# Performance work log

Measured on AMD Instinct MI355X. Metric: run time of the kernel, lower is better.

## Reference

```python
import jax, jax.numpy as jnp
import numpy as np

B, D_IN, H1, H2, LAT, K = 32768, 512, 256, 128, 64, 2048
BN_EPS = 1e-5
COMMIT = 0.25


def _linear_w(k, i, o):
    # xavier-uniform-ish init
    lim = np.sqrt(6.0 / (i + o)).astype(np.float32)
    return jax.random.uniform(k, (i, o), jnp.float32, -lim, lim)


def _bn_params(keys, n):
    g = jax.random.uniform(keys[0], (n,), jnp.float32, 0.5, 1.5)
    b = 0.1 * jax.random.normal(keys[1], (n,), jnp.float32)
    m = 0.1 * jax.random.normal(keys[2], (n,), jnp.float32)
    v = jax.random.uniform(keys[3], (n,), jnp.float32, 0.5, 1.5)
    return g, b, m, v


def setup_inputs() -> dict:
    key = jax.random.key(0)
    ks = jax.random.split(key, 32)
    inp = {"x": jax.random.normal(ks[0], (B, D_IN), jnp.float32)}
    # encoder: 512 -> 256 -> 128 -> 64
    inp["ew1"], inp["eb1"] = _linear_w(ks[1], D_IN, H1), jnp.zeros((H1,), jnp.float32)
    inp["eg1"], inp["ebt1"], inp["em1"], inp["ev1"] = _bn_params(jax.random.split(ks[2], 4), H1)
    inp["ew2"], inp["eb2"] = _linear_w(ks[3], H1, H2), jnp.zeros((H2,), jnp.float32)
    inp["eg2"], inp["ebt2"], inp["em2"], inp["ev2"] = _bn_params(jax.random.split(ks[4], 4), H2)
    inp["ew3"], inp["eb3"] = _linear_w(ks[5], H2, LAT), jnp.zeros((LAT,), jnp.float32)
    # codebook (num_embeddings, latent_dim)
    inp["codebook"] = _linear_w(ks[6], K, LAT).reshape(K, LAT)
    # decoder: 64 -> 128 -> 256 -> 512
    inp["dw1"], inp["db1"] = _linear_w(ks[7], LAT, H2), jnp.zeros((H2,), jnp.float32)
    inp["dg1"], inp["dbt1"], inp["dm1"], inp["dv1"] = _bn_params(jax.random.split(ks[8], 4), H2)
    inp["dw2"], inp["db2"] = _linear_w(ks[9], H2, H1), jnp.zeros((H1,), jnp.float32)
    inp["dg2"], inp["dbt2"], inp["dm2"], inp["dv2"] = _bn_params(jax.random.split(ks[10], 4), H1)
    inp["dw3"], inp["db3"] = _linear_w(ks[11], H1, D_IN), jnp.zeros((D_IN,), jnp.float32)
    return inp


def _bn(x, g, b, m, v):
    # BatchNorm1d in eval mode: running stats
    return (x - m) * (g * jax.lax.rsqrt(v + BN_EPS)) + b


def reference(x, ew1, eb1, eg1, ebt1, em1, ev1,
              ew2, eb2, eg2, ebt2, em2, ev2,
              ew3, eb3, codebook,
              dw1, db1, dg1, dbt1, dm1, dv1,
              dw2, db2, dg2, dbt2, dm2, dv2,
              dw3, db3):
    # ---- encoder MLP (Dropout is identity in eval) ----
    h = _bn(jax.nn.relu(x @ ew1 + eb1), eg1, ebt1, em1, ev1)
    h = _bn(jax.nn.relu(h @ ew2 + eb2), eg2, ebt2, em2, ev2)
    z_e = h @ ew3 + eb3  # [B, LAT]

    # ---- vector quantization: cdist + argmin + gather ----
    # squared L2 distance (argmin-equivalent to cdist p=2)
    d2 = (jnp.sum(z_e * z_e, axis=1, keepdims=True)
          + jnp.sum(codebook * codebook, axis=1)[None, :]
          - 2.0 * (z_e @ codebook.T))  # [B, K]
    idx = jnp.argmin(d2, axis=-1)  # [B]
    z_q = codebook[idx]  # gather, [B, LAT]

    codebook_loss = jnp.mean((z_q - jax.lax.stop_gradient(z_e)) ** 2)
    commit_loss = jnp.mean((z_e - jax.lax.stop_gradient(z_q)) ** 2)
    vq_loss = codebook_loss + COMMIT * commit_loss

    # straight-through estimator
    z_q = z_e + jax.lax.stop_gradient(z_q - z_e)

    # ---- decoder MLP ----
    h = _bn(jax.nn.relu(z_q @ dw1 + db1), dg1, dbt1, dm1, dv1)
    h = _bn(jax.nn.relu(h @ dw2 + db2), dg2, dbt2, dm2, dv2)
    x_recon = h @ dw3 + db3  # [B, D_IN]

    recon_err = jnp.mean((x_recon - x) ** 2)
    return x_recon, vq_loss, idx, recon_err
```

## Files before the change

### kernel.cpp

```cpp
#include <hip/hip_runtime.h>

#define B_ROWS 32768
#define D_IN   512
#define H1_N   256
#define H2_N   128
#define LAT_N  64
#define K_CB   2048

#define BN 128
#define BK 32

#define VQ_MARGIN 4.0e-3f

typedef __attribute__((ext_vector_type(8))) short s8v;
typedef __attribute__((ext_vector_type(4))) float f4v;

__device__ inline unsigned short f2bf(float f) {
    union { float f; unsigned u; } v; v.f = f;
    unsigned r = v.u + 0x7fffu + ((v.u >> 16) & 1u);
    return (unsigned short)(r >> 16);
}
__device__ inline float bf2f(unsigned short h) {
    union { unsigned u; float f; } v; v.u = ((unsigned)h) << 16;
    return v.f;
}

#define SWZ(row) ((((row) >> 2) & 7) << 3)

__global__ __launch_bounds__(128, 2) void gemm_f32_wide(
    const float* __restrict__ A, const float* __restrict__ W,
    const float* __restrict__ bias,
    const float* __restrict__ bn_g, const float* __restrict__ bn_b,
    const float* __restrict__ bn_m, const float* __restrict__ bn_v,
    float* __restrict__ out, int M, int N)
{
    __shared__ float sA[BK][128];
    __shared__ float sB[BK][BN];
    const int tid = threadIdx.x;
    const int tr = tid >> 4;
    const int tc = tid & 15;
    const int row0 = blockIdx.x * 128;
    const int n0   = blockIdx.y * BN;

    float acc[16][8];
#pragma unroll
    for (int i = 0; i < 16; ++i)
#pragma unroll
        for (int j = 0; j < 8; ++j) acc[i][j] = 0.f;

    for (int k0 = 0; k0 < M; k0 += BK) {
#pragma unroll
        for (int it = 0; it < 8; ++it) {
            int s = tid + it * 128;
            int m = s >> 3;
            int kq = s & 7;
            float4 v = *reinterpret_cast<const float4*>(
                &A[(size_t)(row0 + m) * M + k0 + kq * 4]);
            int kk = kq * 4;
            sA[kk + 0][m ^ SWZ(kk + 0)] = v.x;
            sA[kk + 1][m ^ SWZ(kk + 1)] = v.y;
            sA[kk + 2][m ^ SWZ(kk + 2)] = v.z;
            sA[kk + 3][m ^ SWZ(kk + 3)] = v.w;
        }
#pragma unroll
        for (int it = 0; it < 8; ++it) {
            int s = tid + it * 128;
            int k = s >> 5;
            int nq = s & 31;
            float4 v = *reinterpret_cast<const float4*>(
                &W[(size_t)(k0 + k) * N + n0 + nq * 4]);
            *reinterpret_cast<float4*>(&sB[k][nq * 4]) = v;
        }
        __syncthreads();
#pragma unroll 4
        for (int k = 0; k < BK; ++k) {
            int b0a = (tr * 16) ^ SWZ(k);
            int b1a = (tr * 16 + 8) ^ SWZ(k);
            float a[16];
            {
                float4 v0 = *reinterpret_cast<float4*>(&sA[k][b0a]);
                float4 v1 = *reinterpret_cast<float4*>(&sA[k][b0a + 4]);
                float4 v2 = *reinterpret_cast<float4*>(&sA[k][b1a]);
                float4 v3 = *reinterpret_cast<float4*>(&sA[k][b1a + 4]);
                a[0]=v0.x; a[1]=v0.y; a[2]=v0.z; a[3]=v0.w;
                a[4]=v1.x; a[5]=v1.y; a[6]=v1.z; a[7]=v1.w;
                a[8]=v2.x; a[9]=v2.y; a[10]=v2.z; a[11]=v2.w;
                a[12]=v3.x; a[13]=v3.y; a[14]=v3.z; a[15]=v3.w;
            }
            float4 c0 = *reinterpret_cast<float4*>(&sB[k][tc * 4]);
            float4 c1 = *reinterpret_cast<float4*>(&sB[k][64 + tc * 4]);
            float b[8] = {c0.x, c0.y, c0.z, c0.w, c1.x, c1.y, c1.z, c1.w};
#pragma unroll
            for (int i = 0; i < 16; ++i)
#pragma unroll
                for (int j = 0; j < 8; ++j)
                    acc[i][j] = fmaf(a[i], b[j], acc[i][j]);
        }
        __syncthreads();
    }

    const int nb0 = n0 + tc * 4;
    const int nb1 = n0 + 64 + tc * 4;
    float bi[8], sc[8], sh[8];
#pragma unroll
    for (int g = 0; g < 2; ++g) {
        int nb = g ? nb1 : nb0;
#pragma unroll
        for (int j = 0; j < 4; ++j) {
            int n = nb + j;
            bi[g * 4 + j] = bias[n];
            float s = bn_g[n] * rsqrtf(bn_v[n] + 1e-5f);
            sc[g * 4 + j] = s;
            sh[g * 4 + j] = bn_b[n] - bn_m[n] * s;
        }
    }
#pragma unroll
    for (int i = 0; i < 16; ++i) {
        int row = row0 + tr * 16 + i;
#pragma unroll
        for (int g = 0; g < 2; ++g) {
            int nb = g ? nb1 : nb0;
            float o[4];
#pragma unroll
            for (int j = 0; j < 4; ++j) {
                float v = acc[i][g * 4 + j] + bi[g * 4 + j];
                v = v > 0.f ? v : 0.f;
                v = v * sc[g * 4 + j] + sh[g * 4 + j];
                o[j] = v;
            }
            *reinterpret_cast<float4*>(&out[(size_t)row * N + nb]) =
                make_float4(o[0], o[1], o[2], o[3]);
        }
    }
}

template <int MODE>
__global__ __launch_bounds__(256, 6) void gemm_fused(
    const float* __restrict__ A, const float* __restrict__ W,
    const float* __restrict__ bias,
    const float* __restrict__ bn_g, const float* __restrict__ bn_b,
    const float* __restrict__ bn_m, const float* __restrict__ bn_v,
    float* __restrict__ out, int M, int N)
{
    __shared__ float sA[BK][64];
    __shared__ float sB[BK][BN];
    const int tid = threadIdx.x;
    const int tr = tid >> 4;
    const int tc = tid & 15;
    const int row0 = blockIdx.x * 64;
    const int n0   = blockIdx.y * BN;

    float acc[4][8];
#pragma unroll
    for (int i = 0; i < 4; ++i)
#pragma unroll
        for (int j = 0; j < 8; ++j) acc[i][j] = 0.f;

    for (int k0 = 0; k0 < M; k0 += BK) {
#pragma unroll
        for (int it = 0; it < 2; ++it) {
            int s = tid + it * 256;
            int m = s >> 3;
            int kq = s & 7;
            float4 v = *reinterpret_cast<const float4*>(
                &A[(size_t)(row0 + m) * M + k0 + kq * 4]);
            int kk = kq * 4;
            sA[kk + 0][m ^ SWZ(kk + 0)] = v.x;
            sA[kk + 1][m ^ SWZ(kk + 1)] = v.y;
            sA[kk + 2][m ^ SWZ(kk + 2)] = v.z;
            sA[kk + 3][m ^ SWZ(kk + 3)] = v.w;
        }
#pragma unroll
        for (int it = 0; it < 4; ++it) {
            int s = tid + it * 256;
            int k = s >> 5;
            int nq = s & 31;
            int n = n0 + nq * 4;
            float4 v = make_float4(0.f, 0.f, 0.f, 0.f);
            if (n < N)
                v = *reinterpret_cast<const float4*>(&W[(size_t)(k0 + k) * N + n]);
            *reinterpret_cast<float4*>(&sB[k][nq * 4]) = v;
        }
        __syncthreads();
#pragma unroll 4
        for (int k = 0; k < BK; ++k) {
            int ac = (tr * 4) ^ SWZ(k);
            float4 a0 = *reinterpret_cast<float4*>(&sA[k][ac]);
            float a[4] = {a0.x, a0.y, a0.z, a0.w};
            float4 b0 = *reinterpret_cast<float4*>(&sB[k][tc * 4]);
            float4 b1 = *reinterpret_cast<float4*>(&sB[k][64 + tc * 4]);
            float b[8] = {b0.x, b0.y, b0.z, b0.w, b1.x, b1.y, b1.z, b1.w};
#pragma unroll
            for (int i = 0; i < 4; ++i)
#pragma unroll
                for (int j = 0; j < 8; ++j)
                    acc[i][j] = fmaf(a[i], b[j], acc[i][j]);
        }
        __syncthreads();
    }

    const int nb0 = n0 + tc * 4;
    const int nb1 = n0 + 64 + tc * 4;
    float bi[8], sc[8], sh[8];
#pragma unroll
    for (int g = 0; g < 2; ++g) {
        int nb = g ? nb1 : nb0;
        if (nb < N) {
#pragma unroll
            for (int j = 0; j < 4; ++j) {
                int n = nb + j;
                bi[g * 4 + j] = bias[n];
                if (MODE == 0) {
                    float s = bn_g[n] * rsqrtf(bn_v[n] + 1e-5f);
                    sc[g * 4 + j] = s;
                    sh[g * 4 + j] = bn_b[n] - bn_m[n] * s;
                }
            }
        }
    }
#pragma unroll
    for (int i = 0; i < 4; ++i) {
        int row = row0 + tr * 4 + i;
#pragma unroll
        for (int g = 0; g < 2; ++g) {
            int nb = g ? nb1 : nb0;
            if (nb < N) {
                float o[4];
#pragma unroll
                for (int j = 0; j < 4; ++j) {
                    float v = acc[i][g * 4 + j] + bi[g * 4 + j];
                    if (MODE == 0) {
                        v = v > 0.f ? v : 0.f;
                        v = v * sc[g * 4 + j] + sh[g * 4 + j];
                    }
                    o[j] = v;
                }
                *reinterpret_cast<float4*>(&out[(size_t)row * N + nb]) =
                    make_float4(o[0], o[1], o[2], o[3]);
            }
        }
    }
}

__device__ inline void wprep_body(const float* __restrict__ w,
                                  unsigned short* __restrict__ w_hi,
                                  unsigned short* __restrict__ w_lo,
                                  int K, int N, int idx)
{
    if (idx >= N * K) return;
    int n = idx / K, k = idx - n * K;
    float f = w[(size_t)k * N + n];
    unsigned u = __float_as_uint(f);
    float lo = f - __uint_as_float(u & 0xffff0000u);
    w_hi[idx] = (unsigned short)(u >> 16);
    w_lo[idx] = f2bf(lo);
}

__global__ __launch_bounds__(256) void prep_all(
    const float* __restrict__ dw3, unsigned short* w3hi, unsigned short* w3lo,
    const float* __restrict__ dw2, unsigned short* w2hi, unsigned short* w2lo,
    const float* __restrict__ dw1, unsigned short* w1hi, unsigned short* w1lo,
    const float* __restrict__ cb, unsigned short* cb_hi, unsigned short* cb_lo,
    float* __restrict__ cn, int* __restrict__ rcnt, float* __restrict__ repairp)
{
    int bid = blockIdx.x;
    int tid = threadIdx.x;
    if (bid < 512) {
        wprep_body(dw3, w3hi, w3lo, H1_N, D_IN, bid * 256 + tid);
    } else if (bid < 640) {
        wprep_body(dw2, w2hi, w2lo, H2_N, H1_N, (bid - 512) * 256 + tid);
    } else if (bid < 672) {
        wprep_body(dw1, w1hi, w1lo, LAT_N, H2_N, (bid - 640) * 256 + tid);
    } else {
        int blk = bid - 672;
        if (blk == 0) {
            if (tid == 0) rcnt[0] = 0;
            repairp[tid] = 0.f;
        }
        int j = blk * 256 + tid;
        float s = 0.f;
#pragma unroll
        for (int lq = 0; lq < 16; ++lq) {
            float4 v = *reinterpret_cast<const float4*>(&cb[(size_t)j * LAT_N + lq * 4]);
            float e[4] = {v.x, v.y, v.z, v.w};
            ushort4 h, l;
            unsigned short* hp = &h.x;
            unsigned short* lp = &l.x;
#pragma unroll
            for (int t = 0; t < 4; ++t) {
                s = fmaf(e[t], e[t], s);
                unsigned short hb = f2bf(e[t]);
                hp[t] = hb;
                lp[t] = f2bf(e[t] - bf2f(hb));
            }
            *reinterpret_cast<ushort4*>(&cb_hi[(size_t)j * LAT_N + lq * 4]) = h;
            *reinterpret_cast<ushort4*>(&cb_lo[(size_t)j * LAT_N + lq * 4]) = l;
        }
        cn[j] = s;
    }
}

template <int MODE, int K>
__global__ __launch_bounds__(256, 2) void mfma_gemm(
    const unsigned short* __restrict__ A_hi,
    const unsigned short* __restrict__ A_lo,
    const unsigned short* __restrict__ w_hi,
    const unsigned short* __restrict__ w_lo,
    const float* __restrict__ bias,
    const float* __restrict__ bn_g, const float* __restrict__ bn_b,
    const float* __restrict__ bn_m, const float* __restrict__ bn_v,
    unsigned short* __restrict__ out_hi, unsigned short* __restrict__ out_lo,
    float* __restrict__ out_f32,
    const float* __restrict__ xref, float* __restrict__ partials, int N)
{
    const int lane = threadIdx.x & 63;
    const int wv = threadIdx.x >> 6;
    const int wr = wv >> 1, wc = wv & 1;
    const int rbase = blockIdx.x * 128 + wr * 64;
    const int cbase = blockIdx.y * 128 + wc * 64;
    const int lr = lane & 15, lg = lane >> 4;

    f4v acc[4][4];
#pragma unroll
    for (int rt = 0; rt < 4; ++rt)
#pragma unroll
        for (int ct = 0; ct < 4; ++ct)
            acc[rt][ct] = (f4v){0.f, 0.f, 0.f, 0.f};

#pragma unroll
    for (int ks = 0; ks < K / 32; ++ks) {
        s8v ah[4], al[4], bh[4], bl[4];
#pragma unroll
        for (int rt = 0; rt < 4; ++rt) {
            size_t off = (size_t)(rbase + rt * 16 + lr) * K + ks * 32 + lg * 8;
            ah[rt] = *reinterpret_cast<const s8v*>(&A_hi[off]);
            al[rt] = *reinterpret_cast<const s8v*>(&A_lo[off]);
        }
#pragma unroll
        for (int ct = 0; ct < 4; ++ct) {
            size_t off = (size_t)(cbase + ct * 16 + lr) * K + ks * 32 + lg * 8;
            bh[ct] = *reinterpret_cast<const s8v*>(&w_hi[off]);
            bl[ct] = *reinterpret_cast<const s8v*>(&w_lo[off]);
        }
#pragma unroll
        for (int rt = 0; rt < 4; ++rt)
#pragma unroll
            for (int ct = 0; ct < 4; ++ct) {
                acc[rt][ct] = __builtin_amdgcn_mfma_f32_16x16x32_bf16(
                    ah[rt], bh[ct], acc[rt][ct], 0, 0, 0);
                acc[rt][ct] = __builtin_amdgcn_mfma_f32_16x16x32_bf16(
                    al[rt], bh[ct], acc[rt][ct], 0, 0, 0);
                acc[rt][ct] = __builtin_amdgcn_mfma_f32_16x16x32_bf16(
                    ah[rt], bl[ct], acc[rt][ct], 0, 0, 0);
            }
    }

    float sq = 0.f;
#pragma unroll
    for (int ct = 0; ct < 4; ++ct) {
        int col = cbase + ct * 16 + lr;
        float bi = bias[col];
        float sc = 0.f, sh = 0.f;
        if (MODE == 0) {
            float s = bn_g[col] * rsqrtf(bn_v[col] + 1e-5f);
            sc = s;
            sh = bn_b[col] - bn_m[col] * s;
        }
#pragma unroll
        for (int rt = 0; rt < 4; ++rt)
#pragma unroll
            for (int i = 0; i < 4; ++i) {
                int row = rbase + rt * 16 + lg * 4 + i;
                float v = acc[rt][ct][i] + bi;
                if (MODE == 0) {
                    v = fmaxf(v, 0.f) * sc + sh;
                    unsigned u = __float_as_uint(v);
                    out_hi[(size_t)row * N + col] = (unsigned short)(u >> 16);
                    out_lo[(size_t)row * N + col] =
                        f2bf(v - __uint_as_float(u & 0xffff0000u));
                }
                if (MODE == 2) {
                    float d = v - xref[(size_t)row * N + col];
                    sq = fmaf(d, d, sq);
                    out_f32[(size_t)row * N + col] = v;
                }
            }
    }
    if (MODE == 2) {
        __shared__ float red[256];
        red[threadIdx.x] = sq;
        __syncthreads();
        for (int off = 128; off > 0; off >>= 1) {
            if (threadIdx.x < off) red[threadIdx.x] += red[threadIdx.x + off];
            __syncthreads();
        }
        if (threadIdx.x == 0)
            partials[blockIdx.y * gridDim.x + blockIdx.x] = red[0];
    }
}

__global__ __launch_bounds__(256) void vq_mfma(
    const float* __restrict__ z, const unsigned short* __restrict__ cb_hi,
    const unsigned short* __restrict__ cb_lo, const float* __restrict__ cnorm,
    float4* __restrict__ cand)
{
    const int lane = threadIdx.x & 63;
    const int wid  = blockIdx.x * 4 + (threadIdx.x >> 6);
    const int rbase = (wid >> 3) * 64;
    const int cblk  = wid & 7;
    const int cbase = cblk * 256;
    const int lr = lane & 15;
    const int lg = lane >> 4;

    s8v a_hi[4][2], a_lo[4][2];
#pragma unroll
    for (int rt = 0; rt < 4; ++rt) {
        int row = rbase + rt * 16 + lr;
#pragma unroll
        for (int ks = 0; ks < 2; ++ks) {
            const float* p = &z[(size_t)row * LAT_N + ks * 32 + lg * 8];
            float4 v0 = *reinterpret_cast<const float4*>(p);
            float4 v1 = *reinterpret_cast<const float4*>(p + 4);
            float vv[8] = {v0.x, v0.y, v0.z, v0.w, v1.x, v1.y, v1.z, v1.w};
#pragma unroll
            for (int jj = 0; jj < 8; ++jj) {
                unsigned short hb = f2bf(vv[jj]);
                a_hi[rt][ks][jj] = (short)hb;
                a_lo[rt][ks][jj] = (short)f2bf(vv[jj] - bf2f(hb));
            }
        }
    }

    float b1[4][4], b2[4][4];
    int j1[4][4];
#pragma unroll
    for (int rt = 0; rt < 4; ++rt)
#pragma unroll
        for (int i = 0; i < 4; ++i) {
            b1[rt][i] = 3.4e38f; b2[rt][i] = 3.4e38f; j1[rt][i] = 0;
        }

    for (int ct = 0; ct < 16; ++ct) {
        int col = cbase + ct * 16 + lr;
        const unsigned short* ph = &cb_hi[(size_t)col * LAT_N + lg * 8];
        const unsigned short* pl = &cb_lo[(size_t)col * LAT_N + lg * 8];
        s8v bh0 = *reinterpret_cast<const s8v*>(ph);
        s8v bh1 = *reinterpret_cast<const s8v*>(ph + 32);
        s8v bl0 = *reinterpret_cast<const s8v*>(pl);
        s8v bl1 = *reinterpret_cast<const s8v*>(pl + 32);
        float cn = cnorm[col];
#pragma unroll
        for (int rt = 0; rt < 4; ++rt) {
            f4v acc = {0.f, 0.f, 0.f, 0.f};
            acc = __builtin_amdgcn_mfma_f32_16x16x32_bf16(a_hi[rt][0], bh0, acc, 0, 0, 0);
            acc = __builtin_amdgcn_mfma_f32_16x16x32_bf16(a_hi[rt][1], bh1, acc, 0, 0, 0);
            acc = __builtin_amdgcn_mfma_f32_16x16x32_bf16(a_lo[rt][0], bh0, acc, 0, 0, 0);
            acc = __builtin_amdgcn_mfma_f32_16x16x32_bf16(a_lo[rt][1], bh1, acc, 0, 0, 0);
            acc = __builtin_amdgcn_mfma_f32_16x16x32_bf16(a_hi[rt][0], bl0, acc, 0, 0, 0);
            acc = __builtin_amdgcn_mfma_f32_16x16x32_bf16(a_hi[rt][1], bl1, acc, 0, 0, 0);
#pragma unroll
            for (int i = 0; i < 4; ++i) {
                float d = fmaf(-2.f, acc[i], cn);
// ... 68 lines not shown
    float sq = 0.f;
    if (b2 - b1 >= VQ_MARGIN) {
#pragma unroll
        for (int lq = 0; lq < 16; ++lq) {
            float4 cv = *reinterpret_cast<const float4*>(&cb[(size_t)j1 * LAT_N + lq * 4]);
            float4 zv = *reinterpret_cast<const float4*>(&z[(size_t)row * LAT_N + lq * 4]);
            float d0 = cv.x - zv.x, d1 = cv.y - zv.y;
            float d2 = cv.z - zv.z, d3 = cv.w - zv.w;
            sq = fmaf(d0, d0, sq); sq = fmaf(d1, d1, sq);
            sq = fmaf(d2, d2, sq); sq = fmaf(d3, d3, sq);
        }
        const uint4* gh = reinterpret_cast<const uint4*>(&cbhi[(size_t)j1 * LAT_N]);
        const uint4* gl = reinterpret_cast<const uint4*>(&cblo[(size_t)j1 * LAT_N]);
        uint4* dh = reinterpret_cast<uint4*>(&zqhi[(size_t)row * LAT_N]);
        uint4* dl = reinterpret_cast<uint4*>(&zqlo[(size_t)row * LAT_N]);
#pragma unroll
        for (int q = 0; q < 8; ++q) { dh[q] = gh[q]; dl[q] = gl[q]; }
    } else {
        int s = atomicAdd(rcnt, 1);
        if (s < B_ROWS) rlist[s] = row;
    }
    red[tid] = sq;
    __syncthreads();
    for (int off = 128; off > 0; off >>= 1) {
        if (tid < off) red[tid] += red[tid + off];
        __syncthreads();
    }
    if (tid == 0) mergep[blockIdx.x] = red[0];
}

#define RB 8
__global__ __launch_bounds__(256) void vq_repair(
    const int* __restrict__ rcnt, const int* __restrict__ rlist,
    const float* __restrict__ z, const float* __restrict__ cb,
    const float* __restrict__ cn,
    const unsigned short* __restrict__ cbhi,
    const unsigned short* __restrict__ cblo,
    unsigned short* __restrict__ zqhi, unsigned short* __restrict__ zqlo,
    float* __restrict__ idxf, float* __restrict__ repairp)
{
    __shared__ float sz[RB][LAT_N];
    __shared__ float rv[256];
    __shared__ int ri[256];
    const int tid = threadIdx.x;
    const int count = min(rcnt[0], B_ROWS);
    if (blockIdx.x * RB >= count) return;
    float lsum = 0.f;
    for (int base = blockIdx.x * RB; base < count; base += gridDim.x * RB) {
        int nr = min(RB, count - base);
        __syncthreads();
        for (int s = tid; s < nr * LAT_N; s += 256) {
            int r = s >> 6, d = s & 63;
            int rr = rlist[base + r];
            rr = ((unsigned)rr < (unsigned)B_ROWS) ? rr : 0;
            sz[r][d] = z[(size_t)rr * LAT_N + d];
        }
        __syncthreads();
        float bv[RB];
        int bj[RB];
#pragma unroll
        for (int r = 0; r < RB; ++r) { bv[r] = 3.4e38f; bj[r] = 0; }
        for (int k = 0; k < K_CB / 256; ++k) {
            int cidx = tid + k * 256;
            float acc[RB];
#pragma unroll
            for (int r = 0; r < RB; ++r) acc[r] = 0.f;
            const float* cp = &cb[(size_t)cidx * LAT_N];
#pragma unroll 2
            for (int d4 = 0; d4 < 16; ++d4) {
                float4 cv = *reinterpret_cast<const float4*>(cp + d4 * 4);
#pragma unroll
                for (int r = 0; r < RB; ++r) {
                    acc[r] = fmaf(sz[r][d4 * 4 + 0], cv.x, acc[r]);
                    acc[r] = fmaf(sz[r][d4 * 4 + 1], cv.y, acc[r]);
                    acc[r] = fmaf(sz[r][d4 * 4 + 2], cv.z, acc[r]);
                    acc[r] = fmaf(sz[r][d4 * 4 + 3], cv.w, acc[r]);
                }
            }
            float cnv = cn[cidx];
#pragma unroll
            for (int r = 0; r < RB; ++r) {
                float d = fmaf(-2.f, acc[r], cnv);
                if (d < bv[r] || (d == bv[r] && cidx < bj[r])) {
                    bv[r] = d; bj[r] = cidx;
                }
            }
        }
        for (int r = 0; r < RB; ++r) {
            if (r >= nr) break;
            rv[tid] = bv[r];
            ri[tid] = bj[r];
            __syncthreads();
            for (int off = 128; off > 0; off >>= 1) {
                if (tid < off) {
                    float ov = rv[tid + off];
                    int oi = ri[tid + off];
                    if (ov < rv[tid] || (ov == rv[tid] && oi < ri[tid])) {
                        rv[tid] = ov; ri[tid] = oi;
                    }
                }
                __syncthreads();
            }
            int bjf = ri[0];
            int rr = rlist[base + r];
            bool ok = (unsigned)rr < (unsigned)B_ROWS;
            rr = ok ? rr : 0;
            if (tid == 0 && ok) idxf[rr] = (float)bjf;
            float v = 0.f;
            if (tid < 64) {
                float d = cb[(size_t)bjf * LAT_N + tid] - sz[r][tid];
                v = d * d;
            }
            __syncthreads();
            rv[tid] = v;
            __syncthreads();
// ... 77 lines not shown
    const float* dg2  = (const float*)d_in[24];
    const float* dbt2 = (const float*)d_in[25];
    const float* dm2  = (const float*)d_in[26];
    const float* dv2  = (const float*)d_in[27];
    const float* dw3  = (const float*)d_in[28];
    const float* db3  = (const float*)d_in[29];

    float* outf = (float*)d_out;
    const size_t XR_OFF = 0;
    const size_t VQ_OFF = (size_t)B_ROWS * D_IN;
    const size_t IDX_OFF = VQ_OFF + 1;
    const size_t RE_OFF = IDX_OFF + B_ROWS;

    float* wsf = (float*)d_ws;
    size_t off = 0;
    float* buf256 = wsf + off; off += (size_t)B_ROWS * H1_N;
    float* buf128 = wsf + off; off += (size_t)B_ROWS * H2_N;
    float* zbuf   = wsf + off; off += (size_t)B_ROWS * LAT_N;
    float* cnbuf  = wsf + off; off += K_CB;
    float* mergep = wsf + off; off += 128;
    float* repairp= wsf + off; off += 256;
    float* rep    = wsf + off; off += 1024;
    unsigned short* cbhi = (unsigned short*)(wsf + off); off += K_CB * LAT_N / 2;
    unsigned short* cblo = (unsigned short*)(wsf + off); off += K_CB * LAT_N / 2;
    float4* candb = (float4*)(wsf + off); off += (size_t)B_ROWS * 8 * 4;
    int* rcnt  = (int*)(wsf + off); off += 16;
    int* rlist = (int*)(wsf + off); off += B_ROWS;
    unsigned short* w1hi = (unsigned short*)(wsf + off); off += (H2_N * LAT_N) / 2;
    unsigned short* w1lo = (unsigned short*)(wsf + off); off += (H2_N * LAT_N) / 2;
    unsigned short* w2hi = (unsigned short*)(wsf + off); off += (H1_N * H2_N) / 2;
    unsigned short* w2lo = (unsigned short*)(wsf + off); off += (H1_N * H2_N) / 2;
    unsigned short* w3hi = (unsigned short*)(wsf + off); off += (D_IN * H1_N) / 2;
    unsigned short* w3lo = (unsigned short*)(wsf + off); off += (D_IN * H1_N) / 2;
    unsigned short* zqhi = (unsigned short*)(wsf + off); off += (size_t)B_ROWS * LAT_N / 2;
    unsigned short* zqlo = (unsigned short*)(wsf + off); off += (size_t)B_ROWS * LAT_N / 2;

    unsigned short* h1hi = (unsigned short*)buf128;
    unsigned short* h1lo = (unsigned short*)(buf128 + (size_t)B_ROWS * 64);
    unsigned short* h2hi = (unsigned short*)buf256;
    unsigned short* h2lo = (unsigned short*)(buf256 + (size_t)B_ROWS * 128);

    dim3 blk(256);

    prep_all<<<dim3(680), blk, 0, stream>>>(
        dw3, w3hi, w3lo, dw2, w2hi, w2lo, dw1, w1hi, w1lo,
        cb, cbhi, cblo, cnbuf, rcnt, repairp);

    gemm_f32_wide<<<dim3(B_ROWS / 128, H1_N / BN), dim3(128), 0, stream>>>(
        x, ew1, eb1, eg1, ebt1, em1, ev1, buf256, D_IN, H1_N);
    gemm_fused<0><<<dim3(B_ROWS / 64, 1), blk, 0, stream>>>(
        buf256, ew2, eb2, eg2, ebt2, em2, ev2, buf128, H1_N, H2_N);
    gemm_fused<1><<<dim3(B_ROWS / 64, 1), blk, 0, stream>>>(
        buf128, ew3, eb3, nullptr, nullptr, nullptr, nullptr, zbuf, H2_N, LAT_N);

    vq_mfma<<<dim3(1024), blk, 0, stream>>>(zbuf, cbhi, cblo, cnbuf, candb);
    vq_merge<<<dim3(B_ROWS / 256), blk, 0, stream>>>(
        candb, zbuf, cb, cbhi, cblo, zqhi, zqlo,
        outf + IDX_OFF, rlist, rcnt, mergep);
    vq_repair<<<dim3(256), blk, 0, stream>>>(
        rcnt, rlist, zbuf, cb, cnbuf, cbhi, cblo, zqhi, zqlo,
        outf + IDX_OFF, repairp);

    mfma_gemm<0, LAT_N><<<dim3(B_ROWS / 128, H2_N / 128), blk, 0, stream>>>(
        zqhi, zqlo, w1hi, w1lo, db1, dg1, dbt1, dm1, dv1,
        h1hi, h1lo, nullptr, nullptr, nullptr, H2_N);
    mfma_gemm<0, H2_N><<<dim3(B_ROWS / 128, H1_N / 128), blk, 0, stream>>>(
        h1hi, h1lo, w2hi, w2lo, db2, dg2, dbt2, dm2, dv2,
        h2hi, h2lo, nullptr, nullptr, nullptr, H1_N);
    mfma_gemm<2, H1_N><<<dim3(B_ROWS / 128, D_IN / 128), blk, 0, stream>>>(
        h2hi, h2lo, w3hi, w3lo, db3, nullptr, nullptr, nullptr, nullptr,
        nullptr, nullptr, outf + XR_OFF, x, rep, D_IN);

    finalize_kernel<<<dim3(1), blk, 0, stream>>>(
        mergep, 128, repairp, 256, rep, 1024, outf + VQ_OFF, outf + RE_OFF);
}
```

Before: 479.8 us.

## Move encoder GEMMs to split-bf16 MFMA and recompute encoder in repair

Replaces the fp32 FMA encoder GEMMs with the existing MFMA kernel, which uses hi/lo bf16 splitting. The first layer splits x into hi/lo on the fly, and the encoder weights are pre-split in prep_all. The last encoder layer also emits z as hi/lo so vq_mfma consumes it directly. The VQ margin is widened, and the repair kernel now recomputes the encoder exactly in fp32 from x for ambiguous rows, which adds repair work whenever more rows fall inside the margin.

```diff
diff --git a/kernel.cpp b/kernel.cpp
--- a/kernel.cpp
+++ b/kernel.cpp
@@ -7,10 +7,7 @@
 #define LAT_N  64
 #define K_CB   2048
 
-#define BN 128
-#define BK 32
-
-#define VQ_MARGIN 4.0e-3f
+#define VQ_MARGIN 6.0e-3f
 
 typedef __attribute__((ext_vector_type(8))) short s8v;
 typedef __attribute__((ext_vector_type(4))) float f4v;
@@ -25,283 +22,9 @@
     return v.f;
 }
 
-#define SWZ(row) ((((row) >> 2) & 7) << 3)
-
-__global__ __launch_bounds__(128, 2) void gemm_f32_wide(
-    const float* __restrict__ A, const float* __restrict__ W,
-    const float* __restrict__ bias,
-    const float* __restrict__ bn_g, const float* __restrict__ bn_b,
-    const float* __restrict__ bn_m, const float* __restrict__ bn_v,
-    float* __restrict__ out, int M, int N)
-{
-    __shared__ float sA[BK][128];
-    __shared__ float sB[BK][BN];
-    const int tid = threadIdx.x;
-    const int tr = tid >> 4;
-    const int tc = tid & 15;
-    const int row0 = blockIdx.x * 128;
-    const int n0   = blockIdx.y * BN;
-
-    float acc[16][8];
-#pragma unroll
-    for (int i = 0; i < 16; ++i)
-#pragma unroll
-        for (int j = 0; j < 8; ++j) acc[i][j] = 0.f;
-
-    for (int k0 = 0; k0 < M; k0 += BK) {
-#pragma unroll
-        for (int it = 0; it < 8; ++it) {
-            int s = tid + it * 128;
-            int m = s >> 3;
-            int kq = s & 7;
-            float4 v = *reinterpret_cast<const float4*>(
-                &A[(size_t)(row0 + m) * M + k0 + kq * 4]);
-            int kk = kq * 4;
-            sA[kk + 0][m ^ SWZ(kk + 0)] = v.x;
-            sA[kk + 1][m ^ SWZ(kk + 1)] = v.y;
-            sA[kk + 2][m ^ SWZ(kk + 2)] = v.z;
-            sA[kk + 3][m ^ SWZ(kk + 3)] = v.w;
-        }
-#pragma unroll
-        for (int it = 0; it < 8; ++it) {
-            int s = tid + it * 128;
-            int k = s >> 5;
-            int nq = s & 31;
-            float4 v = *reinterpret_cast<const float4*>(
-                &W[(size_t)(k0 + k) * N + n0 + nq * 4]);
-            *reinterpret_cast<float4*>(&sB[k][nq * 4]) = v;
-        }
-        __syncthreads();
-#pragma unroll 4
-        for (int k = 0; k < BK; ++k) {
-            int b0a = (tr * 16) ^ SWZ(k);
-            int b1a = (tr * 16 + 8) ^ SWZ(k);
-            float a[16];
-            {
-                float4 v0 = *reinterpret_cast<float4*>(&sA[k][b0a]);
-                float4 v1 = *reinterpret_cast<float4*>(&sA[k][b0a + 4]);
-                float4 v2 = *reinterpret_cast<float4*>(&sA[k][b1a]);
-                float4 v3 = *reinterpret_cast<float4*>(&sA[k][b1a + 4]);
-                a[0]=v0.x; a[1]=v0.y; a[2]=v0.z; a[3]=v0.w;
-                a[4]=v1.x; a[5]=v1.y; a[6]=v1.z; a[7]=v1.w;
-                a[8]=v2.x; a[9]=v2.y; a[10]=v2.z; a[11]=v2.w;
-                a[12]=v3.x; a[13]=v3.y; a[14]=v3.z; a[15]=v3.w;
-            }
-            float4 c0 = *reinterpret_cast<float4*>(&sB[k][tc * 4]);
-            float4 c1 = *reinterpret_cast<float4*>(&sB[k][64 + tc * 4]);
-            float b[8] = {c0.x, c0.y, c0.z, c0.w, c1.x, c1.y, c1.z, c1.w};
-#pragma unroll
-            for (int i = 0; i < 16; ++i)
-#pragma unroll
-                for (int j = 0; j < 8; ++j)
-                    acc[i][j] = fmaf(a[i], b[j], acc[i][j]);
-        }
-        __syncthreads();
-    }
-
-    const int nb0 = n0 + tc * 4;
-    const int nb1 = n0 + 64 + tc * 4;
-    float bi[8], sc[8], sh[8];
-#pragma unroll
-    for (int g = 0; g < 2; ++g) {
-        int nb = g ? nb1 : nb0;
-#pragma unroll
-        for (int j = 0; j < 4; ++j) {
-            int n = nb + j;
-            bi[g * 4 + j] = bias[n];
-            float s = bn_g[n] * rsqrtf(bn_v[n] + 1e-5f);
-            sc[g * 4 + j] = s;
-            sh[g * 4 + j] = bn_b[n] - bn_m[n] * s;
-        }
-    }
-#pragma unroll
-    for (int i = 0; i < 16; ++i) {
-        int row = row0 + tr * 16 + i;
-#pragma unroll
-        for (int g = 0; g < 2; ++g) {
-            int nb = g ? nb1 : nb0;
-            float o[4];
-#pragma unroll
-            for (int j = 0; j < 4; ++j) {
-                float v = acc[i][g * 4 + j] + bi[g * 4 + j];
-                v = v > 0.f ? v : 0.f;
-                v = v * sc[g * 4 + j] + sh[g * 4 + j];
-                o[j] = v;
-            }
-            *reinterpret_cast<float4*>(&out[(size_t)row * N + nb]) =
-                make_float4(o[0], o[1], o[2], o[3]);
-        }
-    }
-}
-
-template <int MODE>
-__global__ __launch_bounds__(256, 6) void gemm_fused(
-    const float* __restrict__ A, const float* __restrict__ W,
-    const float* __restrict__ bias,
-    const float* __restrict__ bn_g, const float* __restrict__ bn_b,
-    const float* __restrict__ bn_m, const float* __restrict__ bn_v,
-    float* __restrict__ out, int M, int N)
-{
-    __shared__ float sA[BK][64];
-    __shared__ float sB[BK][BN];
-    const int tid = threadIdx.x;
-    const int tr = tid >> 4;
-    const int tc = tid & 15;
-    const int row0 = blockIdx.x * 64;
-    const int n0   = blockIdx.y * BN;
-
-    float acc[4][8];
-#pragma unroll
-    for (int i = 0; i < 4; ++i)
-#pragma unroll
-        for (int j = 0; j < 8; ++j) acc[i][j] = 0.f;
-
-    for (int k0 = 0; k0 < M; k0 += BK) {
-#pragma unroll
-        for (int it = 0; it < 2; ++it) {
-            int s = tid + it * 256;
-            int m = s >> 3;
-            int kq = s & 7;
-            float4 v = *reinterpret_cast<const float4*>(
-                &A[(size_t)(row0 + m) * M + k0 + kq * 4]);
-            int kk = kq * 4;
-            sA[kk + 0][m ^ SWZ(kk + 0)] = v.x;
-            sA[kk + 1][m ^ SWZ(kk + 1)] = v.y;
-            sA[kk + 2][m ^ SWZ(kk + 2)] = v.z;
-            sA[kk + 3][m ^ SWZ(kk + 3)] = v.w;
-        }
-#pragma unroll
-        for (int it = 0; it < 4; ++it) {
-            int s = tid + it * 256;
-            int k = s >> 5;
-            int nq = s & 31;
-            int n = n0 + nq * 4;
-            float4 v = make_float4(0.f, 0.f, 0.f, 0.f);
-            if (n < N)
-                v = *reinterpret_cast<const float4*>(&W[(size_t)(k0 + k) * N + n]);
-            *reinterpret_cast<float4*>(&sB[k][nq * 4]) = v;
-        }
-        __syncthreads();
-#pragma unroll 4
-        for (int k = 0; k < BK; ++k) {
-            int ac = (tr * 4) ^ SWZ(k);
-            float4 a0 = *reinterpret_cast<float4*>(&sA[k][ac]);
-            float a[4] = {a0.x, a0.y, a0.z, a0.w};
-            float4 b0 = *reinterpret_cast<float4*>(&sB[k][tc * 4]);
-            float4 b1 = *reinterpret_cast<float4*>(&sB[k][64 + tc * 4]);
-            float b[8] = {b0.x, b0.y, b0.z, b0.w, b1.x, b1.y, b1.z, b1.w};
-#pragma unroll
-            for (int i = 0; i < 4; ++i)
-#pragma unroll
-                for (int j = 0; j < 8; ++j)
-                    acc[i][j] = fmaf(a[i], b[j], acc[i][j]);
-        }
-        __syncthreads();
-    }
-
-    const int nb0 = n0 + tc * 4;
-    const int nb1 = n0 + 64 + tc * 4;
-    float bi[8], sc[8], sh[8];
-#pragma unroll
-    for (int g = 0; g < 2; ++g) {
-        int nb = g ? nb1 : nb0;
-        if (nb < N) {
-#pragma unroll
-            for (int j = 0; j < 4; ++j) {
-                int n = nb + j;
-                bi[g * 4 + j] = bias[n];
-                if (MODE == 0) {
-                    float s = bn_g[n] * rsqrtf(bn_v[n] + 1e-5f);
-                    sc[g * 4 + j] = s;
-                    sh[g * 4 + j] = bn_b[n] - bn_m[n] * s;
-                }
-            }
-        }
-    }
-#pragma unroll
-    for (int i = 0; i < 4; ++i) {
-        int row = row0 + tr * 4 + i;
-#pragma unroll
-        for (int g = 0; g < 2; ++g) {
-            int nb = g ? nb1 : nb0;
-            if (nb < N) {
-                float o[4];
-#pragma unroll
-                for (int j = 0; j < 4; ++j) {
-                    float v = acc[i][g * 4 + j] + bi[g * 4 + j];
-                    if (MODE == 0) {
-                        v = v > 0.f ? v : 0.f;
-                        v = v * sc[g * 4 + j] + sh[g * 4 + j];
-                    }
-                    o[j] = v;
-                }
-                *reinterpret_cast<float4*>(&out[(size_t)row * N + nb]) =
-                    make_float4(o[0], o[1], o[2], o[3]);
-            }
-        }
-    }
-}
-
-__device__ inline void wprep_body(const float* __restrict__ w,
-                                  unsigned short* __restrict__ w_hi,
-                                  unsigned short* __restrict__ w_lo,
-                                  int K, int N, int idx)
-{
-    if (idx >= N * K) return;
-    int n = idx / K, k = idx - n * K;
-    float f = w[(size_t)k * N + n];
-    unsigned u = __float_as_uint(f);
-    float lo = f - __uint_as_float(u & 0xffff0000u);
-    w_hi[idx] = (unsigned short)(u >> 16);
-    w_lo[idx] = f2bf(lo);
-}
-
-__global__ __launch_bounds__(256) void prep_all(
-    const float* __restrict__ dw3, unsigned short* w3hi, unsigned short* w3lo,
-    const float* __restrict__ dw2, unsigned short* w2hi, unsigned short* w2lo,
-    const float* __restrict__ dw1, unsigned short* w1hi, unsigned short* w1lo,
-    const float* __restrict__ cb, unsigned short* cb_hi, unsigned short* cb_lo,
-    float* __restrict__ cn, int* __restrict__ rcnt, float* __restrict__ repairp)
-{
-    int bid = blockIdx.x;
-    int tid = threadIdx.x;
-    if (bid < 512) {
-        wprep_body(dw3, w3hi, w3lo, H1_N, D_IN, bid * 256 + tid);
-    } else if (bid < 640) {
-        wprep_body(dw2, w2hi, w2lo, H2_N, H1_N, (bid - 512) * 256 + tid);
-    } else if (bid < 672) {
-        wprep_body(dw1, w1hi, w1lo, LAT_N, H2_N, (bid - 640) * 256 + tid);
-    } else {
-        int blk = bid - 672;
-        if (blk == 0) {
-            if (tid == 0) rcnt[0] = 0;
-            repairp[tid] = 0.f;
-        }
-        int j = blk * 256 + tid;
-        float s = 0.f;
-#pragma unroll
-        for (int lq = 0; lq < 16; ++lq) {
-            float4 v = *reinterpret_cast<const float4*>(&cb[(size_t)j * LAT_N + lq * 4]);
-            float e[4] = {v.x, v.y, v.z, v.w};
-            ushort4 h, l;
-            unsigned short* hp = &h.x;
-            unsigned short* lp = &l.x;
-#pragma unroll
-            for (int t = 0; t < 4; ++t) {
-                s = fmaf(e[t], e[t], s);
-                unsigned short hb = f2bf(e[t]);
-                hp[t] = hb;
-                lp[t] = f2bf(e[t] - bf2f(hb));
-            }
-            *reinterpret_cast<ushort4*>(&cb_hi[(size_t)j * LAT_N + lq * 4]) = h;
-            *reinterpret_cast<ushort4*>(&cb_lo[(size_t)j * LAT_N + lq * 4]) = l;
-        }
-        cn[j] = s;
-    }
-}
-
-template <int MODE, int K>
+template <int MODE, int K, int CT, bool ASPLIT>
 __global__ __launch_bounds__(256, 2) void mfma_gemm(
+    const float* __restrict__ A_f32,
     const unsigned short* __restrict__ A_hi,
     const unsigned short* __restrict__ A_lo,
     const unsigned short* __restrict__ w_hi,
@@ -317,27 +40,48 @@
     const int wv = threadIdx.x >> 6;
     const int wr = wv >> 1, wc = wv & 1;
     const int rbase = blockIdx.x * 128 + wr * 64;
-    const int cbase = blockIdx.y * 128 + wc * 64;
+    const int cbase = blockIdx.y * (32 * CT) + wc * (16 * CT);
     const int lr = lane & 15, lg = lane >> 4;
 
-    f4v acc[4][4];
+    f4v acc[4][CT];
 #pragma unroll
     for (int rt = 0; rt < 4; ++rt)
 #pragma unroll
-        for (int ct = 0; ct < 4; ++ct)
+        for (int ct = 0; ct < CT; ++ct)
             acc[rt][ct] = (f4v){0.f, 0.f, 0.f, 0.f};
 
-#pragma unroll
     for (int ks = 0; ks < K / 32; ++ks) {
-        s8v ah[4], al[4], bh[4], bl[4];
+        s8v ah[4], al[4], bh[CT], bl[CT];
 #pragma unroll
         for (int rt = 0; rt < 4; ++rt) {
             size_t off = (size_t)(rbase + rt * 16 + lr) * K + ks * 32 + lg * 8;
-            ah[rt] = *reinterpret_cast<const s8v*>(&A_hi[off]);
-            al[rt] = *reinterpret_cast<const s8v*>(&A_lo[off]);
-        }
-#pragma unroll
-        for (int ct = 0; ct < 4; ++ct) {
+            if constexpr (ASPLIT) {
+                const float* p = &A_f32[off];
+                float4 v0 = *reinterpret_cast<const float4*>(p);
+                float4 v1 = *reinterpret_cast<const float4*>(p + 4);
+                float fv[8] = {v0.x, v0.y, v0.z, v0.w, v1.x, v1.y, v1.z, v1.w};
+                unsigned uu[8], llv[8];
+#pragma unroll
+                for (int j = 0; j < 8; ++j) {
+                    uu[j] = __float_as_uint(fv[j]);
+                    float lo = fv[j] - __uint_as_float(uu[j] & 0xffff0000u);
+                    llv[j] = __float_as_uint(lo);
+                }
+                union { s8v v; unsigned w[4]; } H, L;
+#pragma unroll
+                for (int m = 0; m < 4; ++m) {
+                    H.w[m] = __builtin_amdgcn_perm(uu[2 * m + 1], uu[2 * m], 0x07060302u);
+                    L.w[m] = __builtin_amdgcn_perm(llv[2 * m + 1], llv[2 * m], 0x07060302u);
+                }
+                ah[rt] = H.v;
+                al[rt] = L.v;
+            } else {
+                ah[rt] = *reinterpret_cast<const s8v*>(&A_hi[off]);
+                al[rt] = *reinterpret_cast<const s8v*>(&A_lo[off]);
+            }
+        }
+#pragma unroll
+        for (int ct = 0; ct < CT; ++ct) {
             size_t off = (size_t)(cbase + ct * 16 + lr) * K + ks * 32 + lg * 8;
             bh[ct] = *reinterpret_cast<const s8v*>(&w_hi[off]);
             bl[ct] = *reinterpret_cast<const s8v*>(&w_lo[off]);
@@ -345,7 +89,7 @@
 #pragma unroll
         for (int rt = 0; rt < 4; ++rt)
 #pragma unroll
-            for (int ct = 0; ct < 4; ++ct) {
+            for (int ct = 0; ct < CT; ++ct) {
                 acc[rt][ct] = __builtin_amdgcn_mfma_f32_16x16x32_bf16(
                     ah[rt], bh[ct], acc[rt][ct], 0, 0, 0);
                 acc[rt][ct] = __builtin_amdgcn_mfma_f32_16x16x32_bf16(
@@ -357,7 +101,7 @@
 
     float sq = 0.f;
 #pragma unroll
-    for (int ct = 0; ct < 4; ++ct) {
+    for (int ct = 0; ct < CT; ++ct) {
         int col = cbase + ct * 16 + lr;
         float bi = bias[col];
         float sc = 0.f, sh = 0.f;
@@ -372,8 +116,8 @@
             for (int i = 0; i < 4; ++i) {
                 int row = rbase + rt * 16 + lg * 4 + i;
                 float v = acc[rt][ct][i] + bi;
-                if (MODE == 0) {
-                    v = fmaxf(v, 0.f) * sc + sh;
+                if (MODE == 0) v = fmaxf(v, 0.f) * sc + sh;
+                if (MODE == 0 || MODE == 3) {
                     unsigned u = __float_as_uint(v);
                     out_hi[(size_t)row * N + col] = (unsigned short)(u >> 16);
                     out_lo[(size_t)row * N + col] =
@@ -382,8 +126,9 @@
                 if (MODE == 2) {
                     float d = v - xref[(size_t)row * N + col];
                     sq = fmaf(d, d, sq);
+                }
+                if (MODE == 2 || MODE == 3)
                     out_f32[(size_t)row * N + col] = v;
-                }
             }
     }
     if (MODE == 2) {
@@ -399,8 +144,76 @@
     }
 }
 
+__device__ inline void wprep_body(const float* __restrict__ w,
+                                  unsigned short* __restrict__ w_hi,
+                                  unsigned short* __restrict__ w_lo,
+                                  int K, int N, int idx)
+{
+    if (idx >= N * K) return;
+    int n = idx / K, k = idx - n * K;
+    float f = w[(size_t)k * N + n];
+    unsigned u = __float_as_uint(f);
+    float lo = f - __uint_as_float(u & 0xffff0000u);
+    w_hi[idx] = (unsigned short)(u >> 16);
+    w_lo[idx] = f2bf(lo);
+}
+
+__global__ __launch_bounds__(256) void prep_all(
+    const float* __restrict__ dw3, unsigned short* w3hi, unsigned short* w3lo,
+    const float* __restrict__ dw2, unsigned short* w2hi, unsigned short* w2lo,
+    const float* __restrict__ dw1, unsigned short* w1hi, unsigned short* w1lo,
+    const float* __restrict__ ew1, unsigned short* e1hi, unsigned short* e1lo,
+    const float* __restrict__ ew2, unsigned short* e2hi, unsigned short* e2lo,
+    const float* __restrict__ ew3, unsigned short* e3hi, unsigned short* e3lo,
+    const float* __restrict__ cb, unsigned short* cb_hi, unsigned short* cb_lo,
+    float* __restrict__ cn, int* __restrict__ rcnt, float* __restrict__ repairp)
+{
+    int bid = blockIdx.x;
+    int tid = threadIdx.x;
+    if (bid < 512) {
+        wprep_body(dw3, w3hi, w3lo, H1_N, D_IN, bid * 256 + tid);
+    } else if (bid < 640) {
+        wprep_body(dw2, w2hi, w2lo, H2_N, H1_N, (bid - 512) * 256 + tid);
+    } else if (bid < 672) {
+        wprep_body(dw1, w1hi, w1lo, LAT_N, H2_N, (bid - 640) * 256 + tid);
+    } else if (bid < 1184) {
+        wprep_body(ew1, e1hi, e1lo, D_IN, H1_N, (bid - 672) * 256 + tid);
+    } else if (bid < 1312) {
+        wprep_body(ew2, e2hi, e2lo, H1_N, H2_N, (bid - 1184) * 256 + tid);
+    } else if (bid < 1344) {
+        wprep_body(ew3, e3hi, e3lo, H2_N, LAT_N, (bid - 1312) * 256 + tid);
+    } else {
+        int blk = bid - 1344;
+        if (blk == 0) {
+            if (tid == 0) rcnt[0] = 0;
+            repairp[tid] = 0.f;
+        }
+        int j = blk * 256 + tid;
+        float s = 0.f;
+#pragma unroll
+        for (int lq = 0; lq < 16; ++lq) {
+            float4 v = *reinterpret_cast<const float4*>(&cb[(size_t)j * LAT_N + lq * 4]);
+            float e[4] = {v.x, v.y, v.z, v.w};
+            ushort4 h, l;
+            unsigned short* hp = &h.x;
+            unsigned short* lp = &l.x;
+#pragma unroll
+            for (int t = 0; t < 4; ++t) {
+                s = fmaf(e[t], e[t], s);
+                unsigned short hb = f2bf(e[t]);
+                hp[t] = hb;
+                lp[t] = f2bf(e[t] - bf2f(hb));
+            }
+            *reinterpret_cast<ushort4*>(&cb_hi[(size_t)j * LAT_N + lq * 4]) = h;
+            *reinterpret_cast<ushort4*>(&cb_lo[(size_t)j * LAT_N + lq * 4]) = l;
+        }
+        cn[j] = s;
+    }
+}
+
 __global__ __launch_bounds__(256) void vq_mfma(
-    const float* __restrict__ z, const unsigned short* __restrict__ cb_hi,
+    const unsigned short* __restrict__ zhi, const unsigned short* __restrict__ zlo,
+    const unsigned short* __restrict__ cb_hi,
     const unsigned short* __restrict__ cb_lo, const float* __restrict__ cnorm,
     float4* __restrict__ cand)
 {
@@ -418,16 +231,9 @@
         int row = rbase + rt * 16 + lr;
 #pragma unroll
         for (int ks = 0; ks < 2; ++ks) {
-            const float* p = &z[(size_t)row * LAT_N + ks * 32 + lg * 8];
-            float4 v0 = *reinterpret_cast<const float4*>(p);
-            float4 v1 = *reinterpret_cast<const float4*>(p + 4);
-            float vv[8] = {v0.x, v0.y, v0.z, v0.w, v1.x, v1.y, v1.z, v1.w};
-#pragma unroll
-            for (int jj = 0; jj < 8; ++jj) {
-                unsigned short hb = f2bf(vv[jj]);
-                a_hi[rt][ks][jj] = (short)hb;
-                a_lo[rt][ks][jj] = (short)f2bf(vv[jj] - bf2f(hb));
-            }
+            size_t off = (size_t)row * LAT_N + ks * 32 + lg * 8;
+            a_hi[rt][ks] = *reinterpret_cast<const s8v*>(&zhi[off]);
+            a_lo[rt][ks] = *reinterpret_cast<const s8v*>(&zlo[off]);
         }
     }
 
@@ -562,13 +368,23 @@
 #define RB 8
 __global__ __launch_bounds__(256) void vq_repair(
     const int* __restrict__ rcnt, const int* __restrict__ rlist,
-    const float* __restrict__ z, const float* __restrict__ cb,
-    const float* __restrict__ cn,
+    const float* __restrict__ x,
+    const float* __restrict__ ew1, const float* __restrict__ eb1,
+    const float* __restrict__ eg1, const float* __restrict__ ebt1,
+    const float* __restrict__ em1, const float* __restrict__ ev1,
+    const float* __restrict__ ew2, const float* __restrict__ eb2,
+    const float* __restrict__ eg2, const float* __restrict__ ebt2,
+    const float* __restrict__ em2, const float* __restrict__ ev2,
+    const float* __restrict__ ew3, const float* __restrict__ eb3,
+    const float* __restrict__ cb, const float* __restrict__ cn,
     const unsigned short* __restrict__ cbhi,
     const unsigned short* __restrict__ cblo,
     unsigned short* __restrict__ zqhi, unsigned short* __restrict__ zqlo,
     float* __restrict__ idxf, float* __restrict__ repairp)
 {
+    __shared__ float sx[RB][D_IN];
+    __shared__ float sh1[RB][H1_N];
+    __shared__ float sh2[RB][H2_N];
     __shared__ float sz[RB][LAT_N];
     __shared__ float rv[256];
     __shared__ int ri[256];
@@ -579,11 +395,61 @@
     for (int base = blockIdx.x * RB; base < count; base += gridDim.x * RB) {
         int nr = min(RB, count - base);
         __syncthreads();
-        for (int s = tid; s < nr * LAT_N; s += 256) {
-            int r = s >> 6, d = s & 63;
+        for (int s = tid; s < nr * (D_IN / 4); s += 256) {
+            int r = s / (D_IN / 4), q = s - r * (D_IN / 4);
             int rr = rlist[base + r];
             rr = ((unsigned)rr < (unsigned)B_ROWS) ? rr : 0;
-            sz[r][d] = z[(size_t)rr * LAT_N + d];
+            *reinterpret_cast<float4*>(&sx[r][q * 4]) =
+                *reinterpret_cast<const float4*>(&x[(size_t)rr * D_IN + q * 4]);
+        }
+        __syncthreads();
+        {
+            float a[RB];
+#pragma unroll
+            for (int r = 0; r < RB; ++r) a[r] = 0.f;
+            for (int k = 0; k < D_IN; ++k) {
+                float w = ew1[(size_t)k * H1_N + tid];
+#pragma unroll
+                for (int r = 0; r < RB; ++r) a[r] = fmaf(sx[r][k], w, a[r]);
+            }
+            float s1 = eg1[tid] * rsqrtf(ev1[tid] + 1e-5f);
+            float t1 = ebt1[tid] - em1[tid] * s1;
+            float bv = eb1[tid];
+#pragma unroll
+            for (int r = 0; r < RB; ++r) {
+                float h = fmaxf(a[r] + bv, 0.f);
+                sh1[r][tid] = h * s1 + t1;
+            }
+        }
+        __syncthreads();
+        {
+            int c = tid & 127, rg = (tid >> 7) * 4;
+            float a[4] = {0.f, 0.f, 0.f, 0.f};
+            for (int k = 0; k < H1_N; ++k) {
+                float w = ew2[(size_t)k * H2_N + c];
+#pragma unroll
+                for (int r = 0; r < 4; ++r) a[r] = fmaf(sh1[rg + r][k], w, a[r]);
+            }
+            float s2 = eg2[c] * rsqrtf(ev2[c] + 1e-5f);
+            float t2 = ebt2[c] - em2[c] * s2;
+            float bv = eb2[c];
+#pragma unroll
+            for (int r = 0; r < 4; ++r) {
+                float h = fmaxf(a[r] + bv, 0.f);
+                sh2[rg + r][c] = h * s2 + t2;
+            }
+        }
+        __syncthreads();
+        {
+            int c = tid & 63, rg = (tid >> 6) * 2;
+            float a0 = 0.f, a1 = 0.f;
+            for (int k = 0; k < H2_N; ++k) {
+                float w = ew3[(size_t)k * LAT_N + c];
+                a0 = fmaf(sh2[rg][k], w, a0);
+                a1 = fmaf(sh2[rg + 1][k], w, a1);
+            }
+            sz[rg][c] = a0 + eb3[c];
+            sz[rg + 1][c] = a1 + eb3[c];
         }
         __syncthreads();
         float bv[RB];
@@ -592,25 +458,25 @@
         for (int r = 0; r < RB; ++r) { bv[r] = 3.4e38f; bj[r] = 0; }
         for (int k = 0; k < K_CB / 256; ++k) {
             int cidx = tid + k * 256;
-            float acc[RB];
-#pragma unroll
-            for (int r = 0; r < RB; ++r) acc[r] = 0.f;
+            float a[RB];
+#pragma unroll
+            for (int r = 0; r < RB; ++r) a[r] = 0.f;
             const float* cp = &cb[(size_t)cidx * LAT_N];
 #pragma unroll 2
             for (int d4 = 0; d4 < 16; ++d4) {
                 float4 cv = *reinterpret_cast<const float4*>(cp + d4 * 4);
 #pragma unroll
                 for (int r = 0; r < RB; ++r) {
-                    acc[r] = fmaf(sz[r][d4 * 4 + 0], cv.x, acc[r]);
-                    acc[r] = fmaf(sz[r][d4 * 4 + 1], cv.y, acc[r]);
-                    acc[r] = fmaf(sz[r][d4 * 4 + 2], cv.z, acc[r]);
-                    acc[r] = fmaf(sz[r][d4 * 4 + 3], cv.w, acc[r]);
+                    a[r] = fmaf(sz[r][d4 * 4 + 0], cv.x, a[r]);
+                    a[r] = fmaf(sz[r][d4 * 4 + 1], cv.y, a[r]);
+                    a[r] = fmaf(sz[r][d4 * 4 + 2], cv.z, a[r]);
+                    a[r] = fmaf(sz[r][d4 * 4 + 3], cv.w, a[r]);
                 }
             }
             float cnv = cn[cidx];
 #pragma unroll
             for (int r = 0; r < RB; ++r) {
-                float d = fmaf(-2.f, acc[r], cnv);
+                float d = fmaf(-2.f, a[r], cnv);
                 if (d < bv[r] || (d == bv[r] && cidx < bj[r])) {
                     bv[r] = d; bj[r] = cidx;
                 }
@@ -754,43 +620,63 @@
     unsigned short* w2lo = (unsigned short*)(wsf + off); off += (H1_N * H2_N) / 2;
     unsigned short* w3hi = (unsigned short*)(wsf + off); off += (D_IN * H1_N) / 2;
     unsigned short* w3lo = (unsigned short*)(wsf + off); off += (D_IN * H1_N) / 2;
+    unsigned short* e1hi = (unsigned short*)(wsf + off); off += (D_IN * H1_N) / 2;
+    unsigned short* e1lo = (unsigned short*)(wsf + off); off += (D_IN * H1_N) / 2;
+    unsigned short* e2hi = (unsigned short*)(wsf + off); off += (H1_N * H2_N) / 2;
+    unsigned short* e2lo = (unsigned short*)(wsf + off); off += (H1_N * H2_N) / 2;
+    unsigned short* e3hi = (unsigned short*)(wsf + off); off += (H2_N * LAT_N) / 2;
+    unsigned short* e3lo = (unsigned short*)(wsf + off); off += (H2_N * LAT_N) / 2;
     unsigned short* zqhi = (unsigned short*)(wsf + off); off += (size_t)B_ROWS * LAT_N / 2;
     unsigned short* zqlo = (unsigned short*)(wsf + off); off += (size_t)B_ROWS * LAT_N / 2;
 
-    unsigned short* h1hi = (unsigned short*)buf128;
-    unsigned short* h1lo = (unsigned short*)(buf128 + (size_t)B_ROWS * 64);
-    unsigned short* h2hi = (unsigned short*)buf256;
-    unsigned short* h2lo = (unsigned short*)(buf256 + (size_t)B_ROWS * 128);
+    unsigned short* eh1hi = (unsigned short*)buf256;
+    unsigned short* eh1lo = (unsigned short*)(buf256 + (size_t)B_ROWS * 128);
+    unsigned short* zhi   = (unsigned short*)buf256;
+    unsigned short* zlo   = (unsigned short*)(buf256 + (size_t)B_ROWS * 32);
+    unsigned short* dh2hi = (unsigned short*)buf256;
+    unsigned short* dh2lo = (unsigned short*)(buf256 + (size_t)B_ROWS * 128);
+    unsigned short* eh2hi = (unsigned short*)buf128;
+    unsigned short* eh2lo = (unsigned short*)(buf128 + (size_t)B_ROWS * 64);
+    unsigned short* dh1hi = (unsigned short*)buf128;
+    unsigned short* dh1lo = (unsigned short*)(buf128 + (size_t)B_ROWS * 64);
 
     dim3 blk(256);
-
-    prep_all<<<dim3(680), blk, 0, stream>>>(
+    const int GXM = B_ROWS / 128;
+
+    prep_all<<<dim3(1352), blk, 0, stream>>>(
         dw3, w3hi, w3lo, dw2, w2hi, w2lo, dw1, w1hi, w1lo,
+        ew1, e1hi, e1lo, ew2, e2hi, e2lo, ew3, e3hi, e3lo,
         cb, cbhi, cblo, cnbuf, rcnt, repairp);
 
-    gemm_f32_wide<<<dim3(B_ROWS / 128, H1_N / BN), dim3(128), 0, stream>>>(
-        x, ew1, eb1, eg1, ebt1, em1, ev1, buf256, D_IN, H1_N);
-    gemm_fused<0><<<dim3(B_ROWS / 64, 1), blk, 0, stream>>>(
-        buf256, ew2, eb2, eg2, ebt2, em2, ev2, buf128, H1_N, H2_N);
-    gemm_fused<1><<<dim3(B_ROWS / 64, 1), blk, 0, stream>>>(
-        buf128, ew3, eb3, nullptr, nullptr, nullptr, nullptr, zbuf, H2_N, LAT_N);
-
-    vq_mfma<<<dim3(1024), blk, 0, stream>>>(zbuf, cbhi, cblo, cnbuf, candb);
+    mfma_gemm<0, D_IN, 4, true><<<dim3(GXM, H1_N / 128), blk, 0, stream>>>(
+        x, nullptr, nullptr, e1hi, e1lo, eb1, eg1, ebt1, em1, ev1,
+        eh1hi, eh1lo, nullptr, nullptr, nullptr, H1_N);
+    mfma_gemm<0, H1_N, 4, false><<<dim3(GXM, 1), blk, 0, stream>>>(
+        nullptr, eh1hi, eh1lo, e2hi, e2lo, eb2, eg2, ebt2, em2, ev2,
+        eh2hi, eh2lo, nullptr, nullptr, nullptr, H2_N);
+    mfma_gemm<3, H2_N, 2, false><<<dim3(GXM, 1), blk, 0, stream>>>(
+        nullptr, eh2hi, eh2lo, e3hi, e3lo, eb3, nullptr, nullptr, nullptr, nullptr,
+        zhi, zlo, zbuf, nullptr, nullptr, LAT_N);
+
+    vq_mfma<<<dim3(1024), blk, 0, stream>>>(zhi, zlo, cbhi, cblo, cnbuf, candb);
     vq_merge<<<dim3(B_ROWS / 256), blk, 0, stream>>>(
         candb, zbuf, cb, cbhi, cblo, zqhi, zqlo,
         outf + IDX_OFF, rlist, rcnt, mergep);
     vq_repair<<<dim3(256), blk, 0, stream>>>(
-        rcnt, rlist, zbuf, cb, cnbuf, cbhi, cblo, zqhi, zqlo,
+        rcnt, rlist, x,
+        ew1, eb1, eg1, ebt1, em1, ev1,
+        ew2, eb2, eg2, ebt2, em2, ev2,
+        ew3, eb3, cb, cnbuf, cbhi, cblo, zqhi, zqlo,
         outf + IDX_OFF, repairp);
 
-    mfma_gemm<0, LAT_N><<<dim3(B_ROWS / 128, H2_N / 128), blk, 0, stream>>>(
-        zqhi, zqlo, w1hi, w1lo, db1, dg1, dbt1, dm1, dv1,
-        h1hi, h1lo, nullptr, nullptr, nullptr, H2_N);
-    mfma_gemm<0, H2_N><<<dim3(B_ROWS / 128, H1_N / 128), blk, 0, stream>>>(
-        h1hi, h1lo, w2hi, w2lo, db2, dg2, dbt2, dm2, dv2,
-        h2hi, h2lo, nullptr, nullptr, nullptr, H1_N);
-    mfma_gemm<2, H1_N><<<dim3(B_ROWS / 128, D_IN / 128), blk, 0, stream>>>(
-        h2hi, h2lo, w3hi, w3lo, db3, nullptr, nullptr, nullptr, nullptr,
+    mfma_gemm<0, LAT_N, 4, false><<<dim3(GXM, 1), blk, 0, stream>>>(
+        nullptr, zqhi, zqlo, w1hi, w1lo, db1, dg1, dbt1, dm1, dv1,
+        dh1hi, dh1lo, nullptr, nullptr, nullptr, H2_N);
+    mfma_gemm<0, H2_N, 4, false><<<dim3(GXM, H1_N / 128), blk, 0, stream>>>(
+        nullptr, dh1hi, dh1lo, w2hi, w2lo, db2, dg2, dbt2, dm2, dv2,
+        dh2hi, dh2lo, nullptr, nullptr, nullptr, H1_N);
+    mfma_gemm<2, H1_N, 4, false><<<dim3(GXM, D_IN / 128), blk, 0, stream>>>(
+        nullptr, dh2hi, dh2lo, w3hi, w3lo, db3, nullptr, nullptr, nullptr, nullptr,
         nullptr, nullptr, outf + XR_OFF, x, rep, D_IN);
 
     finalize_kernel<<<dim3(1), blk, 0, stream>>>(
```

Result: slower. 501.9 us (+4.6%).
